# Kernel tuning notes

Hardware: AMD Instinct MI355X
Metric: run time of the kernel (lower is better)

The kernel has to match this reference:

```python
import jax, jax.numpy as jnp
import numpy as np
from jax import lax

BN_EPS = 1e-5  # eval-mode BatchNorm with running_mean=0, running_var=1


def _interp_mat(n_in, n_out):
    # align_corners=True bilinear interpolation matrix [n_out, n_in]
    if n_out == 1:
        coords = np.zeros((1,))
    else:
        coords = np.arange(n_out) * (n_in - 1) / (n_out - 1)
    lo = np.clip(np.floor(coords).astype(np.int64), 0, max(n_in - 2, 0))
    frac = (coords - lo).astype(np.float32)
    M = np.zeros((n_out, n_in), dtype=np.float32)
    M[np.arange(n_out), lo] += 1.0 - frac
    if n_in > 1:
        M[np.arange(n_out), lo + 1] += frac
    return jnp.asarray(M)


def _resize_ac(x, H, W):
    # bilinear, align_corners=True, over trailing two dims
    Mh = _interp_mat(x.shape[-2], H)
    Mw = _interp_mat(x.shape[-1], W)
    return jnp.einsum('...hw,Hh,Ww->...HW', x, Mh, Mw)


def _conv(x, w, b, pad):
    y = lax.conv_general_dilated(x, w, (1, 1), [(pad, pad), (pad, pad)],
                                 dimension_numbers=('NCHW', 'OIHW', 'NCHW'))
    return y + b[None, :, None, None]


def setup_inputs() -> dict:
    key = jax.random.key(0)
    ks = jax.random.split(key, 16)
    C, KD, VD, NCLS, BS = 256, 32, 128, 10, 4
    sizes = [64, 32, 16, 8, 4]
    inp = {}
    for l, s in enumerate(sizes):
        inp[f'feat{l}'] = jax.random.normal(ks[l], (BS, C, s, s), jnp.float32)
    inp['attentions'] = jax.random.normal(ks[5], (NCLS, C, 16, 16), jnp.float32)

    def w(k, shape):
        return jax.random.normal(k, shape, jnp.float32) * 0.05

    inp['key_t_w'] = w(ks[6], (KD, C, 3, 3)); inp['key_t_b'] = jnp.zeros((KD,), jnp.float32)
    inp['value_t_w'] = w(ks[7], (VD, C, 3, 3)); inp['value_t_b'] = jnp.zeros((VD,), jnp.float32)
    inp['key_q_w'] = w(ks[8], (5, KD, C, 3, 3)); inp['key_q_b'] = jnp.zeros((5, KD), jnp.float32)
    inp['value_q_w'] = w(ks[9], (5, VD, C, 3, 3)); inp['value_q_b'] = jnp.zeros((5, VD), jnp.float32)
    inp['bn_gamma'] = jnp.ones((5, 256), jnp.float32)
    inp['bn_beta'] = jnp.zeros((5, 256), jnp.float32)
    inp['combine_w'] = w(ks[10], (256, 512, 1, 1)); inp['combine_b'] = jnp.zeros((256,), jnp.float32)
    return inp


def reference(feat0, feat1, feat2, feat3, feat4, attentions,
              key_t_w, key_t_b, value_t_w, value_t_b,
              key_q_w, key_q_b, value_q_w, value_q_b,
              bn_gamma, bn_beta, combine_w, combine_b):
    feats = [feat0, feat1, feat2, feat3, feat4]
    ncls, _, h, w_ = attentions.shape
    hw = h * w_
    kt = _conv(attentions, key_t_w, key_t_b, 1).reshape(ncls, 32, hw)   # [n,32,hw]
    vt = _conv(attentions, value_t_w, value_t_b, 1).reshape(ncls, 128, hw)  # [n,128,hw]
    bn_scale = bn_gamma * np.float32(1.0 / np.sqrt(1.0 + BN_EPS))
    outs, fas = [], []
    for l, f in enumerate(feats):
        bs, _, H, W = f.shape
        fr = _resize_ac(f, h, w_)                                        # [b,C,h,w]
        kq = _conv(fr, key_q_w[l], key_q_b[l], 1).reshape(bs, 32, hw)    # [b,32,hw]
        vq = _conv(fr, value_q_w[l], value_q_b[l], 1)                    # [b,128,h,w]
        # p[b,n,i,j] = sum_k kq[b,k,i] * kt[n,k,j]; softmax over i (torch dim=1)
        p = jnp.einsum('bki,nkj->bnij', kq, kt)
        p = jax.nn.softmax(p, axis=2)
        # full attention maps: channels = template pixel j, spatial = query pixel i
        fa = _resize_ac(jnp.swapaxes(p, 2, 3).reshape(bs, ncls, hw, h, w_), H, W)
        # val_t_out summed over classes: sum_n sum_i vt[n,c,i] * p[b,n,i,j]
        agg = jnp.einsum('nci,bnij->bcj', vt, p).reshape(bs, 128, h, w_)
        final = jnp.concatenate([ncls * vq, agg], axis=1)                # [b,256,h,w]
        final = _resize_ac(final, H, W)
        final = final * bn_scale[l][None, :, None, None] + bn_beta[l][None, :, None, None]
        outs.append(_conv(jnp.concatenate([f, final], axis=1), combine_w, combine_b, 0))
        fas.append(fa)
    return (*outs, *fas)
```

## Files before the change

kernel.cpp:

```cpp
#include <hip/hip_runtime.h>

constexpr int CIN   = 256;
constexpr int KD    = 32;
constexpr int VD    = 128;
constexpr int NCLS  = 10;
constexpr int BS    = 4;
constexpr int HW    = 256;
constexpr float BNC = 0.9999950000374997f;

typedef unsigned short u16;
typedef __attribute__((ext_vector_type(8))) __bf16 bf8v;
typedef __attribute__((ext_vector_type(4))) float f4v;

static __device__ __forceinline__ int imin(int a, int b) { return a < b ? a : b; }

static __device__ __forceinline__ u16 f2bf(float v) {
  union { float f; unsigned u; } x; x.f = v;
  unsigned r = x.u + 0x7FFFu + ((x.u >> 16) & 1u);
  return (u16)(r >> 16);
}
static __device__ __forceinline__ float bf2f(u16 h) {
  union { unsigned u; float f; } x; x.u = ((unsigned)h) << 16;
  return x.f;
}

static __device__ __forceinline__ f4v mfma16(bf8v a, bf8v b, f4v c) {
  return __builtin_amdgcn_mfma_f32_16x16x32_bf16(a, b, c, 0, 0, 0);
}

__constant__ const int c_jbase[5] = {0, 16384, 20480, 21504, 21760};

__global__ __launch_bounds__(256) void k_prep1(
    const float* __restrict__ f0, const float* __restrict__ f1,
    const float* __restrict__ f2, const float* __restrict__ f3,
    const float* __restrict__ f4, const float* __restrict__ att,
    const float* __restrict__ vqw, const float* __restrict__ vtw,
    const float* __restrict__ kqw, const float* __restrict__ ktw,
    const float* __restrict__ cw, const float* __restrict__ gamma,
    const float* __restrict__ cbias, const float* __restrict__ beta,
    u16* __restrict__ Xf, u16* __restrict__ Xr,
    u16* __restrict__ Awv, u16* __restrict__ Awk,
    u16* __restrict__ cwA, u16* __restrict__ cw2A, float* __restrict__ cb) {
  __shared__ float sm[16][65];
  int blk = blockIdx.x;
  int tid = threadIdx.x;
  if (blk < 384) {
    const float* fin; u16* dstbase; int SS, px0;
    if (blk < 344) {
      int l, base, nb;
      if (blk < 256)      { l = 0; base = 0;   nb = 64; }
      else if (blk < 320) { l = 1; base = 256; nb = 16; }
      else if (blk < 336) { l = 2; base = 320; nb = 4; }
      else if (blk < 340) { l = 3; base = 336; nb = 1; }
      else                { l = 4; base = 340; nb = 1; }
      int local = blk - base;
      int b = local / nb, chunk = local % nb;
      int S = 64 >> l; SS = S * S;
      px0 = chunk * 64;
      fin = (l == 0 ? f0 : l == 1 ? f1 : l == 2 ? f2 : l == 3 ? f3 : f4)
            + (size_t)b * CIN * SS;
      dstbase = Xf + (size_t)(c_jbase[l] + b * SS) * 512;
    } else {
      int a = blk - 344;
      int imgA = a >> 2, chunk = a & 3;
      SS = 256; px0 = chunk * 64;
      fin = att + (size_t)imgA * CIN * 256;
      dstbase = Xr + (size_t)(20 + imgA) * 131072;
    }
    int px_r = tid & 63, cr = tid >> 6;
    int px_w = tid >> 2, c4 = (tid & 3) * 4;
    for (int cbk = 0; cbk < 16; ++cbk) {
      __syncthreads();
#pragma unroll
      for (int q = 0; q < 4; ++q) {
        int cl = q * 4 + cr;
        float v = 0.f;
        if (px0 + px_r < SS) v = fin[(size_t)(cbk * 16 + cl) * SS + px0 + px_r];
        sm[cl][px_r] = v;
      }
      __syncthreads();
      if (px0 + px_w < SS) {
        u16 hh[4], ll[4];
#pragma unroll
        for (int e = 0; e < 4; ++e) {
          float v = sm[c4 + e][px_w];
          hh[e] = f2bf(v); ll[e] = f2bf(v - bf2f(hh[e]));
        }
        uint2 wh, wl;
        wh.x = (unsigned)hh[0] | ((unsigned)hh[1] << 16); wh.y = (unsigned)hh[2] | ((unsigned)hh[3] << 16);
        wl.x = (unsigned)ll[0] | ((unsigned)ll[1] << 16); wl.y = (unsigned)ll[2] | ((unsigned)ll[3] << 16);
        u16* dst = dstbase + (size_t)(px0 + px_w) * 512 + cbk * 16 + c4;
        *reinterpret_cast<uint2*>(dst) = wh;
        *reinterpret_cast<uint2*>(dst + 256) = wl;
      }
    }
  } else if (blk < 1464) {
    int gid = (blk - 384) * 256 + tid;
    int lane = gid & 63;
    int grp = gid >> 6;
    const float* src; u16* dst; int kc;
    if (grp < 3456) {
      kc = grp % 72; int ot = (grp / 72) % 8; int sid = grp / (72 * 8);
      src = (sid < 5 ? vqw + (size_t)sid * VD * 2304 : vtw) + (size_t)(ot * 16 + (lane & 15)) * 2304;
      dst = Awv + (size_t)grp * 1024;
    } else {
      int g2 = grp - 3456;
      kc = g2 % 72; int ot = (g2 / 72) % 2; int sid = g2 / 144;
      src = (sid < 5 ? kqw + (size_t)sid * KD * 2304 : ktw) + (size_t)(ot * 16 + (lane & 15)) * 2304;
      dst = Awk + (size_t)g2 * 1024;
    }
    int q0 = (lane >> 4) * 8;
    int t = kc >> 3, c0 = (kc & 7) * 32;
#pragma unroll
    for (int i = 0; i < 8; ++i) {
      int c = c0 + q0 + i;
      float v = src[c * 9 + t];
      u16 h = f2bf(v);
      dst[lane * 8 + i] = h;
      dst[512 + lane * 8 + i] = f2bf(v - bf2f(h));
    }
  } else if (blk < 1848) {
    int blk2 = blk - 1464;
    if (blk2 < 64) {
      int gid = blk2 * 256 + tid;
      int oc = gid >> 6, c0 = (gid & 63) * 4;
      float4 v = *reinterpret_cast<const float4*>(cw + (size_t)oc * 512 + c0);
      const float* vv = (const float*)&v;
      u16 h[4], l[4];
#pragma unroll
      for (int e = 0; e < 4; ++e) { h[e] = f2bf(vv[e]); l[e] = f2bf(vv[e] - bf2f(h[e])); }
      uint2 wh, wl;
      wh.x = (unsigned)h[0] | ((unsigned)h[1] << 16); wh.y = (unsigned)h[2] | ((unsigned)h[3] << 16);
      wl.x = (unsigned)l[0] | ((unsigned)l[1] << 16); wl.y = (unsigned)l[2] | ((unsigned)l[3] << 16);
      *reinterpret_cast<uint2*>(cwA + (size_t)oc * 256 + c0) = wh;
      *reinterpret_cast<uint2*>(cwA + 65536 + (size_t)oc * 256 + c0) = wl;
    } else {
      int gid = (blk2 - 64) * 256 + tid;
      int l = gid / 16384, rem = gid % 16384;
      int oc = rem >> 6, c0 = (rem & 63) * 4;
      u16 h[4], lo[4];
#pragma unroll
      for (int e = 0; e < 4; ++e) {
        int c = c0 + e;
        float v = cw[(size_t)oc * 512 + 256 + c] * (gamma[l * 256 + c] * BNC);
        h[e] = f2bf(v); lo[e] = f2bf(v - bf2f(h[e]));
      }
      uint2 wh, wl;
      wh.x = (unsigned)h[0] | ((unsigned)h[1] << 16); wh.y = (unsigned)h[2] | ((unsigned)h[3] << 16);
      wl.x = (unsigned)lo[0] | ((unsigned)lo[1] << 16); wl.y = (unsigned)lo[2] | ((unsigned)lo[3] << 16);
      *reinterpret_cast<uint2*>(cw2A + (size_t)l * 65536 + oc * 256 + c0) = wh;
      *reinterpret_cast<uint2*>(cw2A + 327680 + (size_t)l * 65536 + oc * 256 + c0) = wl;
    }
  } else {
    int l = blk - 1848, oc = tid;
    float s = cbias[oc];
    for (int c = 0; c < CIN; ++c)
      s += cw[(size_t)oc * 512 + 256 + c] * beta[l * CIN + c];
    cb[l * CIN + oc] = s;
  }
}

__global__ __launch_bounds__(256) void k_prep_xr(
    const u16* __restrict__ Xf, u16* __restrict__ Xr, u16* __restrict__ zrow) {
  int blk = blockIdx.x;
  int img = blk >> 4, yr = blk & 15;
  int l = img >> 2, b = img & 3;
  int S = 64 >> l, SS = S * S;
  int c = threadIdx.x;
  if (blk == 0) { zrow[c] = 0; zrow[256 + c] = 0; }
  float cyf = (float)(yr * (S - 1)) / 15.0f;
  int ylo = imin((int)cyf, S - 2); float fy = cyf - (float)ylo;
  u16* dst = Xr + ((size_t)img * 256 + yr * 16) * 512;
  const u16* srcb = Xf + (size_t)(c_jbase[l] + b * SS) * 512;
  for (int x = 0; x < 16; ++x) {
    float cxf = (float)(x * (S - 1)) / 15.0f;
    int xlo = imin((int)cxf, S - 2); float fx = cxf - (float)xlo;
    const u16* r00 = srcb + (size_t)(ylo * S + xlo) * 512;
    const u16* r10 = srcb + (size_t)((ylo + 1) * S + xlo) * 512;
    float v00 = bf2f(r00[c]) + bf2f(r00[256 + c]);
    float v01 = bf2f(r00[512 + c]) + bf2f(r00[768 + c]);
    float v10 = bf2f(r10[c]) + bf2f(r10[256 + c]);
    float v11 = bf2f(r10[512 + c]) + bf2f(r10[768 + c]);
    float v = (1.f - fy) * ((1.f - fx) * v00 + fx * v01)
            + fy * ((1.f - fx) * v10 + fx * v11);
    u16 h = f2bf(v);
    dst[x * 512 + c] = h;
    dst[x * 512 + 256 + c] = f2bf(v - bf2f(h));
  }
}

__global__ __launch_bounds__(256) void k_conv_mfma(
    const u16* __restrict__ Xr, const u16* __restrict__ Awv, const u16* __restrict__ Awk,
    const u16* __restrict__ zrow,
    float* __restrict__ kqall, u16* __restrict__ vt2, float* __restrict__ f16v,
    const float* __restrict__ vqb, const float* __restrict__ vtb,
    const float* __restrict__ kqb, const float* __restrict__ ktb) {
  int wid = blockIdx.x * 4 + (threadIdx.x >> 6);
  int lane = threadIdx.x & 63;
  bool isV = wid < 1920;
  int img, ot, yp;
  if (isV) { img = wid >> 6; int r = wid & 63; ot = r >> 3; yp = r & 7; }
  else     { int j = wid - 1920; img = j >> 4; int r = j & 15; ot = r >> 3; yp = r & 7; }
  int wset = img < 20 ? (img >> 2) : 5;

  const u16* Ab = isV ? Awv + ((size_t)(wset * 8 + ot)) * 72 * 1024
                      : Awk + ((size_t)(wset * 2 + ot)) * 72 * 1024;
  const u16* Xb = Xr + (size_t)img * 131072;
  int xcol = lane & 15, kg = lane >> 4;
  int y0 = yp * 2, y1 = y0 + 1;

  f4v acc0 = {0.f, 0.f, 0.f, 0.f}, acc1 = {0.f, 0.f, 0.f, 0.f};
  for (int t = 0; t < 9; ++t) {
    int dy = (t >= 6) ? 2 : (t >= 3 ? 1 : 0);
    int dx = t - dy * 3;
    int yy0 = y0 + dy - 1, yy1 = yy0 + 1;
    int xx = xcol + dx - 1;
    bool xok = (unsigned)xx < 16u;
    const u16* base0 = (xok && (unsigned)yy0 < 16u)
                       ? Xb + (size_t)(yy0 * 16 + xx) * 512 : zrow;
    const u16* base1 = (xok && (unsigned)yy1 < 16u)
                       ? Xb + (size_t)(yy1 * 16 + xx) * 512 : zrow;
    const u16* Xr0 = base0 + kg * 8;
    const u16* Xr1 = base1 + kg * 8;
    const u16* Ak = Ab + (size_t)t * 8 * 1024 + lane * 8;
#pragma unroll
    for (int cc = 0; cc < 8; ++cc) {
      bf8v ah = *reinterpret_cast<const bf8v*>(Ak + cc * 1024);
      bf8v al = *reinterpret_cast<const bf8v*>(Ak + cc * 1024 + 512);
      bf8v bh0 = *reinterpret_cast<const bf8v*>(Xr0 + cc * 32);
      bf8v bl0 = *reinterpret_cast<const bf8v*>(Xr0 + cc * 32 + 256);
      bf8v bh1 = *reinterpret_cast<const bf8v*>(Xr1 + cc * 32);
      bf8v bl1 = *reinterpret_cast<const bf8v*>(Xr1 + cc * 32 + 256);
      acc0 = mfma16(ah, bh0, acc0);
      acc0 = mfma16(ah, bl0, acc0);
      acc0 = mfma16(al, bh0, acc0);
      acc1 = mfma16(ah, bh1, acc1);
      acc1 = mfma16(ah, bl1, acc1);
      acc1 = mfma16(al, bh1, acc1);
    }
  }

  int ocbase = ot * 16;
  if (isV && img >= 20) {
    int n = img - 20;
    u16* d2 = vt2 + ((size_t)n * VD + ocbase) * HW;
#pragma unroll
    for (int i = 0; i < 4; ++i) {
      int ocl = kg * 4 + i;
      float bv = vtb[ocbase + ocl];
      float va = acc0[i] + bv, vb = acc1[i] + bv;
      u16 ha = f2bf(va), hb = f2bf(vb);
      size_t ia = (size_t)ocl * HW + y0 * 16 + xcol;
      size_t ib = (size_t)ocl * HW + y1 * 16 + xcol;
      d2[ia] = ha; d2[ia + 327680] = f2bf(va - bf2f(ha));
      d2[ib] = hb; d2[ib + 327680] = f2bf(vb - bf2f(hb));
    }
    return;
  }
  float scale = 1.f;
  const float* bias;
  float* dst;
  if (isV) { dst = f16v + ((size_t)img * VD + ocbase) * HW; bias = vqb + wset * VD + ocbase; scale = (float)NCLS; }
  else if (img < 20) { dst = kqall + ((size_t)img * KD + ocbase) * HW; bias = kqb + wset * KD + ocbase; }
  else { dst = kqall + (size_t)20 * KD * HW + ((size_t)(img - 20) * KD + ocbase) * HW; bias = ktb + ocbase; }
#pragma unroll
  for (int i = 0; i < 4; ++i) {
    int ocl = kg * 4 + i;
    float bv = bias[ocl];
    dst[(size_t)ocl * HW + y0 * 16 + xcol] = (acc0[i] + bv) * scale;
    dst[(size_t)ocl * HW + y1 * 16 + xcol] = (acc1[i] + bv) * scale;
  }
}

__global__ __launch_bounds__(256) void k_pagg(
    const float* __restrict__ kqall, const u16* __restrict__ vt2,
    u16* __restrict__ pT, float* __restrict__ aggn) {
  int blk = blockIdx.x;
  int l = blk / 320;
  int g = blk % 320;
  int bn = g >> 3, jt = g & 7;
  int b = bn / NCLS, n = bn % NCLS;
  int t = threadIdx.x;
  int iq = t >> 5, jl = t & 31;
  int j = jt * 32 + jl;

  __shared__ float buf[8224];
  __shared__ float red[512];

  const float* ktb = kqall + 20 * KD * HW;
  float ktr[KD];
#pragma unroll
  for (int k = 0; k < KD; ++k) ktr[k] = ktb[((size_t)n * KD + k) * HW + j];
  const float* kqb = kqall + (size_t)(l * 4 + b) * KD * HW;
  for (int s = t; s < KD * HW; s += 256) buf[s] = kqb[s];
  __syncthreads();

  float v[32];
#pragma unroll
  for (int ii = 0; ii < 32; ++ii) v[ii] = 0.f;
  for (int k = 0; k < KD; ++k) {
    float a = ktr[k];
    const float4* q4 = (const float4*)&buf[k * 256 + iq * 32];
#pragma unroll
    for (int q = 0; q < 8; ++q) {
      float4 u = q4[q];
      v[q * 4 + 0] += u.x * a; v[q * 4 + 1] += u.y * a;
      v[q * 4 + 2] += u.z * a; v[q * 4 + 3] += u.w * a;
    }
  }
  float ml = -1e30f;
#pragma unroll
  for (int ii = 0; ii < 32; ++ii) ml = fmaxf(ml, v[ii]);
  float sl = 0.f;
#pragma unroll
  for (int ii = 0; ii < 32; ++ii) sl += __expf(v[ii] - ml);
  red[t] = ml;
  red[256 + t] = sl;
  __syncthreads();
  float M = -1e30f;
#pragma unroll
  for (int q = 0; q < 8; ++q) M = fmaxf(M, red[q * 32 + jl]);
  float Ssum = 0.f;
#pragma unroll
  for (int q = 0; q < 8; ++q) Ssum += red[256 + q * 32 + jl] * __expf(red[q * 32 + jl] - M);
  float inv = 1.0f / Ssum;
  u16 tmp[32];
#pragma unroll
  for (int ii = 0; ii < 32; ++ii) {
    float pv = __expf(v[ii] - M) * inv;
    buf[jl * 257 + iq * 32 + ii] = pv;
    tmp[ii] = f2bf(pv);
  }
  u16* prow = pT + (((size_t)(l * 40 + bn) * 256 + j) << 8) + iq * 32;
#pragma unroll
  for (int q = 0; q < 4; ++q) {
    uint4 w;
    w.x = (unsigned)tmp[q * 8 + 0] | ((unsigned)tmp[q * 8 + 1] << 16);
    w.y = (unsigned)tmp[q * 8 + 2] | ((unsigned)tmp[q * 8 + 3] << 16);
    w.z = (unsigned)tmp[q * 8 + 4] | ((unsigned)tmp[q * 8 + 5] << 16);
    w.w = (unsigned)tmp[q * 8 + 6] | ((unsigned)tmp[q * 8 + 7] << 16);
    reinterpret_cast<uint4*>(prow)[q] = w;
  }
  __syncthreads();

  int w = t >> 6, lane = t & 63;
  int row = lane & 15, kg = lane >> 4;
  f4v acc[2][2] = {{{0.f,0.f,0.f,0.f},{0.f,0.f,0.f,0.f}},
                   {{0.f,0.f,0.f,0.f},{0.f,0.f,0.f,0.f}}};
  for (int kc = 0; kc < 8; ++kc) {
    bf8v ah[2], al[2];
#pragma unroll
    for (int ctl = 0; ctl < 2; ++ctl) {
      int ct = w * 2 + ctl;
      const u16* vh = vt2 + ((size_t)n * VD + ct * 16 + row) * 256 + kc * 32 + kg * 8;
      ah[ctl] = *reinterpret_cast<const bf8v*>(vh);
      al[ctl] = *reinterpret_cast<const bf8v*>(vh + 327680);
    }
#pragma unroll
    for (int jt2 = 0; jt2 < 2; ++jt2) {
      union { u16 u[8]; bf8v v8; } Bh;
#pragma unroll
      for (int e = 0; e < 8; ++e)
        Bh.u[e] = f2bf(buf[(jt2 * 16 + row) * 257 + kc * 32 + kg * 8 + e]);
#pragma unroll
      for (int ctl = 0; ctl < 2; ++ctl) {
        acc[ctl][jt2] = mfma16(ah[ctl], Bh.v8, acc[ctl][jt2]);
        acc[ctl][jt2] = mfma16(al[ctl], Bh.v8, acc[ctl][jt2]);
      }
    }
  }
  float* ab = aggn + (size_t)(l * 40 + bn) * VD * HW;
#pragma unroll
  for (int ctl = 0; ctl < 2; ++ctl)
#pragma unroll
    for (int jt2 = 0; jt2 < 2; ++jt2)
#pragma unroll
      for (int i = 0; i < 4; ++i)
        ab[(size_t)(w * 32 + ctl * 16 + kg * 4 + i) * HW + jt * 32 + jt2 * 16 + row]
            = acc[ctl][jt2][i];
}

__global__ __launch_bounds__(256) void k_fa2(
    const u16* __restrict__ pT, float* __restrict__ out) {
  int blk = blockIdx.x;
  int l = blk / 640;
  int local = blk % 640;
  int bn = local >> 4, jg = local & 15;
  int tid = threadIdx.x;
  __shared__ float ld[16][257];
  {
    int jj = tid >> 4, i0 = (tid & 15) * 16;
    const u16* src = pT + (((size_t)(l * 40 + bn) * 256 + jg * 16 + jj) << 8) + i0;
    const uint4* s4 = reinterpret_cast<const uint4*>(src);
    uint4 w0 = s4[0], w1 = s4[1];
    const unsigned* u0 = (const unsigned*)&w0;
    const unsigned* u1 = (const unsigned*)&w1;
#pragma unroll
    for (int e = 0; e < 4; ++e) {
      ld[jj][i0 + e * 2]     = bf2f((u16)(u0[e] & 0xffff));
      ld[jj][i0 + e * 2 + 1] = bf2f((u16)(u0[e] >> 16));
      ld[jj][i0 + 8 + e * 2]     = bf2f((u16)(u1[e] & 0xffff));
      ld[jj][i0 + 8 + e * 2 + 1] = bf2f((u16)(u1[e] >> 16));
    }
  }
  __syncthreads();

  int S_ = 64 >> l, shift = 6 - l, SS = S_ * S_;
  const size_t fa_off[5] = {5586944, 47529984, 58015744, 60637184, 61292544};
  float* ob = out + fa_off[l] + ((size_t)bn * HW + jg * 16) * SS;
  int tot = SS << 4;
  for (int base = tid * 4; base < tot; base += 1024) {
    int jj = base >> (2 * shift);
    int rest = base & (SS - 1);
    int X0 = rest & (S_ - 1), Y = rest >> shift;
    float cyf = (float)(Y * 15) / (float)(S_ - 1);
    int ylo = imin((int)cyf, 14); float fy = cyf - (float)ylo;
    const float* prow = &ld[jj][0];
    f4v rv;
#pragma unroll
    for (int t4 = 0; t4 < 4; ++t4) {
      int X = X0 + t4;
      float cxf = (float)(X * 15) / (float)(S_ - 1);
      int xlo = imin((int)cxf, 14); float fx = cxf - (float)xlo;
      int i00 = ylo * 16 + xlo;
      float v0 = prow[i00],      v1 = prow[i00 + 1];
      float v2 = prow[i00 + 16], v3 = prow[i00 + 17];
      rv[t4] = (1.f - fy) * ((1.f - fx) * v0 + fx * v1)
             + fy * ((1.f - fx) * v2 + fx * v3);
    }
    __builtin_nontemporal_store(rv, (f4v*)(ob + (size_t)jj * SS + rest));
  }
}

__global__ __launch_bounds__(256) void k_g16f(
    const float* __restrict__ f16v, const float* __restrict__ aggn,
    const u16* __restrict__ cw2A, float* __restrict__ g16_all) {
  int blk = blockIdx.x;
  int ohalf = blk & 1;
  int img = blk >> 5, jc = (blk >> 1) & 15;
  int j0 = jc * 16;
  int l = img >> 2, b = img & 3;
  int tid = threadIdx.x;
  __shared__ __align__(16) u16 fsbh[16][280];
  __shared__ __align__(16) u16 fsbl[16][280];
  int jj = tid & 15;
  int c0 = tid >> 4;
  for (int pass = 0; pass < 16; ++pass) {
    int cc = pass * 16 + c0;
    float v;
    if (cc < 128) {
      v = f16v[((size_t)img * VD + cc) * HW + j0 + jj];
    } else {
      const float* ab = aggn + ((size_t)(l * 40 + b * 10) * VD + cc - 128) * HW + j0 + jj;
      v = 0.f;
#pragma unroll
      for (int n = 0; n < NCLS; ++n) v += ab[(size_t)n * VD * HW];
    }
    u16 h = f2bf(v);
    fsbh[jj][cc] = h;
    fsbl[jj][cc] = f2bf(v - bf2f(h));
  }
  __syncthreads();

  int w = tid >> 6, lane = tid & 63;
  int row = lane & 15, kg = lane >> 4;
#pragma unroll
  for (int q = 0; q < 2; ++q) {
    int ot = ohalf * 8 + w * 2 + q;
    const u16* Ah = cw2A + (size_t)l * 65536 + ((size_t)(ot * 16 + row)) * 256 + kg * 8;
    const u16* Al = Ah + 327680;
    f4v acc = {0.f, 0.f, 0.f, 0.f};
#pragma unroll
    for (int kc = 0; kc < 8; ++kc) {
      bf8v ah = *reinterpret_cast<const bf8v*>(Ah + kc * 32);
      bf8v al = *reinterpret_cast<const bf8v*>(Al + kc * 32);
      bf8v bh = *reinterpret_cast<const bf8v*>(&fsbh[row][kc * 32 + kg * 8]);
      bf8v bl = *reinterpret_cast<const bf8v*>(&fsbl[row][kc * 32 + kg * 8]);
      acc = mfma16(ah, bh, acc);
      acc = mfma16(ah, bl, acc);
      acc = mfma16(al, bh, acc);
    }
#pragma unroll
    for (int i = 0; i < 4; ++i)
      g16_all[((size_t)img * CIN + ot * 16 + kg * 4 + i) * HW + j0 + row] = acc[i];
  }
}

__global__ __launch_bounds__(256) void k_out_final(
    const u16* __restrict__ cwA, const u16* __restrict__ Xf,
    const float* __restrict__ g16_all, const float* __restrict__ cb_all,
    float* __restrict__ out) {
  int wid = blockIdx.x * 4 + (threadIdx.x >> 6);
  int lane = threadIdx.x & 63;
  int pt = wid >> 4, octile = wid & 15;
  int l, lb, tl;
  if (pt < 1024)      { l = 0; lb = 0;    tl = 256; }
  else if (pt < 1280) { l = 1; lb = 1024; tl = 64; }
  else if (pt < 1344) { l = 2; lb = 1280; tl = 16; }
  else if (pt < 1360) { l = 3; lb = 1344; tl = 4; }
  else                { l = 4; lb = 1360; tl = 1; }
  int rem = pt - lb;
  int b = rem / tl;
  int pxin = (rem % tl) * 16;
  const size_t ooff[5] = {0, 4194304, 5242880, 5505024, 5570560};
  int S = 64 >> l, SS = S * S, shift = 6 - l;
  int row = lane & 15, kg = lane >> 4;
  int gpx = c_jbase[l] + b * SS + pxin + row;

  const u16* Ah = cwA + ((size_t)(octile * 16 + row)) * 256 + kg * 8;
  const u16* Al = Ah + 65536;
  const u16* Bh = Xf + (size_t)gpx * 512 + kg * 8;
  const u16* Bl = Bh + 256;
  f4v acc = {0.f, 0.f, 0.f, 0.f};
#pragma unroll
  for (int kc = 0; kc < 8; ++kc) {
    bf8v ah = *reinterpret_cast<const bf8v*>(Ah + kc * 32);
    bf8v al = *reinterpret_cast<const bf8v*>(Al + kc * 32);
    bf8v bh = *reinterpret_cast<const bf8v*>(Bh + kc * 32);
    bf8v bl = *reinterpret_cast<const bf8v*>(Bl + kc * 32);
    acc = mfma16(ah, bh, acc);
    acc = mfma16(ah, bl, acc);
    acc = mfma16(al, bh, acc);
  }

  int px = pxin + row;
  int Xc = px & (S - 1), Y = px >> shift;
  float cyf = (float)(Y * 15) / (float)(S - 1);
  int ylo = imin((int)cyf, 14); float fy = cyf - (float)ylo;
  float cxf = (float)(Xc * 15) / (float)(S - 1);
  int xlo = imin((int)cxf, 14); float fx = cxf - (float)xlo;
  int i00 = ylo * 16 + xlo;
  const float* gbase = g16_all + ((size_t)(l * 4 + b) * CIN + octile * 16 + kg * 4) * HW;
  float* ob = out + ooff[l] + ((size_t)b * CIN + octile * 16) * SS + px;
#pragma unroll
  for (int i = 0; i < 4; ++i) {
    const float* g = gbase + (size_t)i * HW + i00;
    float v0 = g[0], v1 = g[1], v2 = g[16], v3 = g[17];
    float bil = (1.f - fy) * ((1.f - fx) * v0 + fx * v1)
              + fy * ((1.f - fx) * v2 + fx * v3);
    float r = acc[i] + bil + cb_all[l * CIN + octile * 16 + kg * 4 + i];
    __builtin_nontemporal_store(r, ob + (size_t)(kg * 4 + i) * SS);
  }
}

extern "C" void kernel_launch(void* const* d_in, const int* in_sizes, int n_in,
                              void* d_out, int out_size, void* d_ws, size_t ws_size,
                              hipStream_t stream) {
  const float* feat[5];
  for (int l = 0; l < 5; ++l) feat[l] = (const float*)d_in[l];
  const float* att   = (const float*)d_in[5];
  const float* ktw   = (const float*)d_in[6];
  const float* ktb   = (const float*)d_in[7];
  const float* vtw   = (const float*)d_in[8];
  const float* vtb   = (const float*)d_in[9];
  const float* kqw   = (const float*)d_in[10];
  const float* kqb   = (const float*)d_in[11];
  const float* vqw   = (const float*)d_in[12];
  const float* vqb   = (const float*)d_in[13];
  const float* gamma = (const float*)d_in[14];
  const float* beta  = (const float*)d_in[15];
  const float* cw    = (const float*)d_in[16];
  const float* cbias = (const float*)d_in[17];
  float* out = (float*)d_out;

  float* ws    = (float*)d_ws;
  float* kqall = ws;
  float* f16v  = ws + 245760;
  u16*   vt2   = (u16*)(ws + 901120);
  u16*   cwA   = (u16*)(ws + 1228800);
  u16*   cw2A  = (u16*)(ws + 1294336);
  float* cb    = ws + 1622016;
  u16*   Xf    = (u16*)(ws + 1623296);
  float* S0    = ws + 7210240;
  u16*   Awv  = (u16*)S0;
  u16*   Awk  = (u16*)(S0 + 1769472);
  u16*   Xr   = (u16*)(S0 + 2211840);
  u16*   zrow = (u16*)(S0 + 4177920);
  float* aggn    = S0;
  float* g16_all = S0 + 6553600;
  u16*   pT      = (u16*)(S0 + 7864320);

  k_prep1<<<1853, 256, 0, stream>>>(
      feat[0], feat[1], feat[2], feat[3], feat[4], att,
      vqw, vtw, kqw, ktw, cw, gamma, cbias, beta,
      Xf, Xr, Awv, Awk, cwA, cw2A, cb);
  k_prep_xr<<<320, 256, 0, stream>>>(Xf, Xr, zrow);
  k_conv_mfma<<<600, 256, 0, stream>>>(
      Xr, Awv, Awk, zrow, kqall, vt2, f16v, vqb, vtb, kqb, ktb);

  k_pagg<<<1600, 256, 0, stream>>>(kqall, vt2, pT, aggn);
  k_fa2<<<3200, 256, 0, stream>>>(pT, out);

  k_g16f<<<640, 256, 0, stream>>>(f16v, aggn, cw2A, g16_all);
  k_out_final<<<5456, 256, 0, stream>>>(cwA, Xf, g16_all, cb, out);
}
```

Measured before the change: 357.7 us.

## Merge attention-map upsample and output GEMM into one interleaved kernel

Replaces the separate full-attention bilinear upsample kernel and the final combine-conv kernel with a single launch. Blocks alternate between the compute-heavy MFMA output tiles and the store-heavy attention-map upsample tiles, in a 2:1 interleave plus a tail. The aim is to overlap memory-bound writes with compute and drop one launch. The cost is that every block reserves the shared-memory buffer even on the GEMM path, which may lower occupancy, and there is divergence from the branch on block kind.

```diff
diff --git a/kernel.cpp b/kernel.cpp
--- a/kernel.cpp
+++ b/kernel.cpp
@@ -380,58 +380,6 @@
             = acc[ctl][jt2][i];
 }
 
-__global__ __launch_bounds__(256) void k_fa2(
-    const u16* __restrict__ pT, float* __restrict__ out) {
-  int blk = blockIdx.x;
-  int l = blk / 640;
-  int local = blk % 640;
-  int bn = local >> 4, jg = local & 15;
-  int tid = threadIdx.x;
-  __shared__ float ld[16][257];
-  {
-    int jj = tid >> 4, i0 = (tid & 15) * 16;
-    const u16* src = pT + (((size_t)(l * 40 + bn) * 256 + jg * 16 + jj) << 8) + i0;
-    const uint4* s4 = reinterpret_cast<const uint4*>(src);
-    uint4 w0 = s4[0], w1 = s4[1];
-    const unsigned* u0 = (const unsigned*)&w0;
-    const unsigned* u1 = (const unsigned*)&w1;
-#pragma unroll
-    for (int e = 0; e < 4; ++e) {
-      ld[jj][i0 + e * 2]     = bf2f((u16)(u0[e] & 0xffff));
-      ld[jj][i0 + e * 2 + 1] = bf2f((u16)(u0[e] >> 16));
-      ld[jj][i0 + 8 + e * 2]     = bf2f((u16)(u1[e] & 0xffff));
-      ld[jj][i0 + 8 + e * 2 + 1] = bf2f((u16)(u1[e] >> 16));
-    }
-  }
-  __syncthreads();
-
-  int S_ = 64 >> l, shift = 6 - l, SS = S_ * S_;
-  const size_t fa_off[5] = {5586944, 47529984, 58015744, 60637184, 61292544};
-  float* ob = out + fa_off[l] + ((size_t)bn * HW + jg * 16) * SS;
-  int tot = SS << 4;
-  for (int base = tid * 4; base < tot; base += 1024) {
-    int jj = base >> (2 * shift);
-    int rest = base & (SS - 1);
-    int X0 = rest & (S_ - 1), Y = rest >> shift;
-    float cyf = (float)(Y * 15) / (float)(S_ - 1);
-    int ylo = imin((int)cyf, 14); float fy = cyf - (float)ylo;
-    const float* prow = &ld[jj][0];
-    f4v rv;
-#pragma unroll
-    for (int t4 = 0; t4 < 4; ++t4) {
-      int X = X0 + t4;
-      float cxf = (float)(X * 15) / (float)(S_ - 1);
-      int xlo = imin((int)cxf, 14); float fx = cxf - (float)xlo;
-      int i00 = ylo * 16 + xlo;
-      float v0 = prow[i00],      v1 = prow[i00 + 1];
-      float v2 = prow[i00 + 16], v3 = prow[i00 + 17];
-      rv[t4] = (1.f - fy) * ((1.f - fx) * v0 + fx * v1)
-             + fy * ((1.f - fx) * v2 + fx * v3);
-    }
-    __builtin_nontemporal_store(rv, (f4v*)(ob + (size_t)jj * SS + rest));
-  }
-}
-
 __global__ __launch_bounds__(256) void k_g16f(
     const float* __restrict__ f16v, const float* __restrict__ aggn,
     const u16* __restrict__ cw2A, float* __restrict__ g16_all) {
@@ -486,60 +434,119 @@
   }
 }
 
-__global__ __launch_bounds__(256) void k_out_final(
-    const u16* __restrict__ cwA, const u16* __restrict__ Xf,
-    const float* __restrict__ g16_all, const float* __restrict__ cb_all,
-    float* __restrict__ out) {
-  int wid = blockIdx.x * 4 + (threadIdx.x >> 6);
-  int lane = threadIdx.x & 63;
-  int pt = wid >> 4, octile = wid & 15;
-  int l, lb, tl;
-  if (pt < 1024)      { l = 0; lb = 0;    tl = 256; }
-  else if (pt < 1280) { l = 1; lb = 1024; tl = 64; }
-  else if (pt < 1344) { l = 2; lb = 1280; tl = 16; }
-  else if (pt < 1360) { l = 3; lb = 1344; tl = 4; }
-  else                { l = 4; lb = 1360; tl = 1; }
-  int rem = pt - lb;
-  int b = rem / tl;
-  int pxin = (rem % tl) * 16;
+__global__ __launch_bounds__(256) void k_combo(
+    const u16* __restrict__ pT, const u16* __restrict__ cwA,
+    const u16* __restrict__ Xf, const float* __restrict__ g16_all,
+    const float* __restrict__ cb_all, float* __restrict__ out) {
+  const size_t fa_off[5] = {5586944, 47529984, 58015744, 60637184, 61292544};
   const size_t ooff[5] = {0, 4194304, 5242880, 5505024, 5570560};
-  int S = 64 >> l, SS = S * S, shift = 6 - l;
-  int row = lane & 15, kg = lane >> 4;
-  int gpx = c_jbase[l] + b * SS + pxin + row;
-
-  const u16* Ah = cwA + ((size_t)(octile * 16 + row)) * 256 + kg * 8;
-  const u16* Al = Ah + 65536;
-  const u16* Bh = Xf + (size_t)gpx * 512 + kg * 8;
-  const u16* Bl = Bh + 256;
-  f4v acc = {0.f, 0.f, 0.f, 0.f};
-#pragma unroll
-  for (int kc = 0; kc < 8; ++kc) {
-    bf8v ah = *reinterpret_cast<const bf8v*>(Ah + kc * 32);
-    bf8v al = *reinterpret_cast<const bf8v*>(Al + kc * 32);
-    bf8v bh = *reinterpret_cast<const bf8v*>(Bh + kc * 32);
-    bf8v bl = *reinterpret_cast<const bf8v*>(Bl + kc * 32);
-    acc = mfma16(ah, bh, acc);
-    acc = mfma16(ah, bl, acc);
-    acc = mfma16(al, bh, acc);
-  }
-
-  int px = pxin + row;
-  int Xc = px & (S - 1), Y = px >> shift;
-  float cyf = (float)(Y * 15) / (float)(S - 1);
-  int ylo = imin((int)cyf, 14); float fy = cyf - (float)ylo;
-  float cxf = (float)(Xc * 15) / (float)(S - 1);
-  int xlo = imin((int)cxf, 14); float fx = cxf - (float)xlo;
-  int i00 = ylo * 16 + xlo;
-  const float* gbase = g16_all + ((size_t)(l * 4 + b) * CIN + octile * 16 + kg * 4) * HW;
-  float* ob = out + ooff[l] + ((size_t)b * CIN + octile * 16) * SS + px;
-#pragma unroll
-  for (int i = 0; i < 4; ++i) {
-    const float* g = gbase + (size_t)i * HW + i00;
-    float v0 = g[0], v1 = g[1], v2 = g[16], v3 = g[17];
-    float bil = (1.f - fy) * ((1.f - fx) * v0 + fx * v1)
-              + fy * ((1.f - fx) * v2 + fx * v3);
-    float r = acc[i] + bil + cb_all[l * CIN + octile * 16 + kg * 4 + i];
-    __builtin_nontemporal_store(r, ob + (size_t)(kg * 4 + i) * SS);
+  __shared__ float ldp[16][257];
+
+  int blk = blockIdx.x;
+  int kind, unit;
+  if (blk < 8184) {
+    int g = blk / 3, r = blk - g * 3;
+    if (r < 2) { kind = 0; unit = g * 2 + r; }
+    else       { kind = 1; unit = g; }
+  } else { kind = 1; unit = 2728 + (blk - 8184); }
+  int tid = threadIdx.x;
+
+  if (kind == 0) {
+    int wid = unit * 4 + (tid >> 6);
+    int lane = tid & 63;
+    int pt = wid >> 4, octile = wid & 15;
+    int l, lb, tl;
+    if (pt < 1024)      { l = 0; lb = 0;    tl = 256; }
+    else if (pt < 1280) { l = 1; lb = 1024; tl = 64; }
+    else if (pt < 1344) { l = 2; lb = 1280; tl = 16; }
+    else if (pt < 1360) { l = 3; lb = 1344; tl = 4; }
+    else                { l = 4; lb = 1360; tl = 1; }
+    int rem = pt - lb;
+    int b = rem / tl;
+    int pxin = (rem % tl) * 16;
+    int S = 64 >> l, SS = S * S, shift = 6 - l;
+    int row = lane & 15, kg = lane >> 4;
+    int gpx = c_jbase[l] + b * SS + pxin + row;
+
+    const u16* Ah = cwA + ((size_t)(octile * 16 + row)) * 256 + kg * 8;
+    const u16* Al = Ah + 65536;
+    const u16* Bh = Xf + (size_t)gpx * 512 + kg * 8;
+    const u16* Bl = Bh + 256;
+    f4v acc = {0.f, 0.f, 0.f, 0.f};
+#pragma unroll
+    for (int kc = 0; kc < 8; ++kc) {
+      bf8v ah = *reinterpret_cast<const bf8v*>(Ah + kc * 32);
+      bf8v al = *reinterpret_cast<const bf8v*>(Al + kc * 32);
+      bf8v bh = *reinterpret_cast<const bf8v*>(Bh + kc * 32);
+      bf8v bl = *reinterpret_cast<const bf8v*>(Bl + kc * 32);
+      acc = mfma16(ah, bh, acc);
+      acc = mfma16(ah, bl, acc);
+      acc = mfma16(al, bh, acc);
+    }
+
+    int px = pxin + row;
+    int Xc = px & (S - 1), Y = px >> shift;
+    float cyf = (float)(Y * 15) / (float)(S - 1);
+    int ylo = imin((int)cyf, 14); float fy = cyf - (float)ylo;
+    float cxf = (float)(Xc * 15) / (float)(S - 1);
+    int xlo = imin((int)cxf, 14); float fx = cxf - (float)xlo;
+    int i00 = ylo * 16 + xlo;
+    const float* gbase = g16_all + ((size_t)(l * 4 + b) * CIN + octile * 16 + kg * 4) * HW;
+    float* ob = out + ooff[l] + ((size_t)b * CIN + octile * 16) * SS + px;
+#pragma unroll
+    for (int i = 0; i < 4; ++i) {
+      const float* g = gbase + (size_t)i * HW + i00;
+      float v0 = g[0], v1 = g[1], v2 = g[16], v3 = g[17];
+      float bil = (1.f - fy) * ((1.f - fx) * v0 + fx * v1)
+                + fy * ((1.f - fx) * v2 + fx * v3);
+      float r = acc[i] + bil + cb_all[l * CIN + octile * 16 + kg * 4 + i];
+      __builtin_nontemporal_store(r, ob + (size_t)(kg * 4 + i) * SS);
+    }
+  } else {
+    int l = unit / 640;
+    int local = unit % 640;
+    int bn = local >> 4, jg = local & 15;
+    {
+      int jj = tid >> 4, i0 = (tid & 15) * 16;
+      const u16* src = pT + (((size_t)(l * 40 + bn) * 256 + jg * 16 + jj) << 8) + i0;
+      const uint4* s4 = reinterpret_cast<const uint4*>(src);
+      uint4 w0 = s4[0], w1 = s4[1];
+      const unsigned* u0 = (const unsigned*)&w0;
+      const unsigned* u1 = (const unsigned*)&w1;
+#pragma unroll
+      for (int e = 0; e < 4; ++e) {
+        ldp[jj][i0 + e * 2]     = bf2f((u16)(u0[e] & 0xffff));
+        ldp[jj][i0 + e * 2 + 1] = bf2f((u16)(u0[e] >> 16));
+        ldp[jj][i0 + 8 + e * 2]     = bf2f((u16)(u1[e] & 0xffff));
+        ldp[jj][i0 + 8 + e * 2 + 1] = bf2f((u16)(u1[e] >> 16));
+      }
+    }
+    __syncthreads();
+
+    int S_ = 64 >> l, shift = 6 - l, SS = S_ * S_;
+    float* ob = out + fa_off[l] + ((size_t)bn * HW + jg * 16) * SS;
+    int tot = SS << 4;
+    for (int base = tid * 4; base < tot; base += 1024) {
+      int jj = base >> (2 * shift);
+      int rest = base & (SS - 1);
+      int X0 = rest & (S_ - 1), Y = rest >> shift;
+      float cyf = (float)(Y * 15) / (float)(S_ - 1);
+      int ylo = imin((int)cyf, 14); float fy = cyf - (float)ylo;
+      const float* prow = &ldp[jj][0];
+      f4v rv;
+#pragma unroll
+      for (int t4 = 0; t4 < 4; ++t4) {
+        int X = X0 + t4;
+        float cxf = (float)(X * 15) / (float)(S_ - 1);
+        int xlo = imin((int)cxf, 14); float fx = cxf - (float)xlo;
+        int i00 = ylo * 16 + xlo;
+        float v0 = prow[i00],      v1 = prow[i00 + 1];
+        float v2 = prow[i00 + 16], v3 = prow[i00 + 17];
+        rv[t4] = (1.f - fy) * ((1.f - fx) * v0 + fx * v1)
+               + fy * ((1.f - fx) * v2 + fx * v3);
+      }
+      __builtin_nontemporal_store(rv, (f4v*)(ob + (size_t)jj * SS + rest));
+    }
   }
 }
 
@@ -589,8 +596,7 @@
       Xr, Awv, Awk, zrow, kqall, vt2, f16v, vqb, vtb, kqb, ktb);
 
   k_pagg<<<1600, 256, 0, stream>>>(kqall, vt2, pT, aggn);
-  k_fa2<<<3200, 256, 0, stream>>>(pT, out);
 
   k_g16f<<<640, 256, 0, stream>>>(f16v, aggn, cw2A, g16_all);
-  k_out_final<<<5456, 256, 0, stream>>>(cwA, Xf, g16_all, cb, out);
-}
+  k_combo<<<8656, 256, 0, stream>>>(pT, cwA, Xf, g16_all, cb, out);
+}
```

New measurement: 327.8 us (median of 2 runs). 1.09x faster.
